# Performance work log

Measured on AMD Instinct MI355X. Metric: run time of the kernel, lower is better.

## Reference

```python
import jax, jax.numpy as jnp
import numpy as np

BATCH_SIZE = 512
N_PARTS = 4
TEMP_FAC = 0.1
D = 4096
EPS = 1e-6


def _static_indices():
    # bs and factor per the n_parts==4, batch_size!=12 branch
    bs = 4 * BATCH_SIZE
    factor = 10 * N_PARTS
    pos = np.arange(bs)
    active = pos[pos % (3 * N_PARTS) < N_PARTS]            # positions that contribute
    # i1..i6 = (pos + k*n_parts) % bs for k = 0..5
    I = (active[:, None] + np.arange(6)[None, :] * N_PARTS) % bs   # (P, 6)
    # denominator indices removed: (pos + k*n_parts) % bs for k = 0..factor*n_parts-1
    offs = (active[:, None] + np.arange(factor * N_PARTS)[None, :] * N_PARTS) % bs
    M = np.ones((active.shape[0], bs), dtype=np.float32)
    M[np.arange(active.shape[0])[:, None], offs] = 0.0     # (P, bs) denominator mask
    return I, M

_I, _M = _static_indices()
# symmetrical-loss pairs: (i1,i2),(i2,i3),(i1,i4),(i4,i5),(i5,i6),(i2,i5),(i3,i6)
_PAIRS = [(0, 1), (1, 2), (0, 3), (3, 4), (4, 5), (1, 4), (2, 5)]


def setup_inputs() -> dict:
    key = jax.random.key(0)
    reg_pred = jax.random.normal(key, (4 * BATCH_SIZE, D), dtype=jnp.float32)
    return {"reg_pred": reg_pred}


def reference(reg_pred):
    I = jnp.asarray(_I)
    M = jnp.asarray(_M)
    norms = jnp.linalg.norm(reg_pred, axis=1)              # (bs,)
    # torch CosineSimilarity: dot / max(||a||*||b||, eps)
    gram = reg_pred @ reg_pred.T                           # (bs, bs)
    S = gram / jnp.maximum(norms[:, None] * norms[None, :], EPS) / TEMP_FAC
    E = jnp.exp(S)                                         # (bs, bs)
    # denominator exp-sums for each anchor role k at each active position p
    Dsum = jnp.einsum('pkb,pb->pk', E[I], M)               # (P, 6)
    total = jnp.float32(0.0)
    for a, b in _PAIRS:
        num = S[I[:, a], I[:, b]]                          # (P,)
        en = jnp.exp(num)
        total = total + jnp.sum(-jnp.log(en / (en + Dsum[:, a]))
                                - jnp.log(en / (en + Dsum[:, b])))
    return total / (6 * BATCH_SIZE)
```

## Files before the change

### kernel.cpp

```cpp
#include <hip/hip_runtime.h>
#include <hip/hip_bf16.h>
#include <stdint.h>

#define NROWS 2048
#define DIM   4096
#define NACT  684
#define INV_TEMP 10.0f
#define NPANEL 32
#define NTILE64 528
#define NK 64
#define FP8_SCALE 16.0f
#define OUT_SCALE (INV_TEMP / 256.0f)

#define WAITCNT_VM0   0x0F70
#define WAITCNT_VM4   0x0F74
#define WAITCNT_VM8   0x0F78

typedef __attribute__((ext_vector_type(4))) float floatx4;
typedef __attribute__((ext_vector_type(16))) float floatx16;
typedef __attribute__((ext_vector_type(4))) int intx4;
typedef __attribute__((ext_vector_type(8))) int intx8;
typedef __attribute__((ext_vector_type(8))) short shortx8;
typedef __attribute__((ext_vector_type(8))) unsigned short ushortx8;

static __device__ __forceinline__ unsigned short f32_to_bf16(float f) {
  union { float f; unsigned int u; } v; v.f = f;
  unsigned int u = v.u;
  unsigned int r = u + 0x7fffu + ((u >> 16) & 1u);
  return (unsigned short)(r >> 16);
}
static __device__ __forceinline__ float bf16_to_f32(unsigned short u) {
  union { unsigned int u; float f; } v; v.u = ((unsigned int)u) << 16;
  return v.f;
}
static __device__ __forceinline__ unsigned short f32_to_f16(float f) {
  _Float16 h = (_Float16)f;
  union { _Float16 h; unsigned short u; } v; v.h = h;
  return v.u;
}
static __device__ __forceinline__ float f16_to_f32(unsigned short u) {
  union { unsigned short u; _Float16 h; } v; v.u = u;
  return (float)v.h;
}

__global__ __launch_bounds__(256) void k_normconv_fp8(const float* __restrict__ X,
                                                      unsigned char* __restrict__ Yq,
                                                      float* __restrict__ T,
                                                      float* __restrict__ out) {
  const int row = blockIdx.x;
  if (threadIdx.x == 0) T[row] = 0.f;
  if (row == 0 && threadIdx.x == 64) *out = 0.f;
  const float4* xr = (const float4*)(X + (size_t)row * DIM);
  float4 v[4];
  float s = 0.f;
#pragma unroll
  for (int t = 0; t < 4; t++) {
    float4 w = xr[threadIdx.x + t * 256];
    v[t] = w;
    s += w.x * w.x + w.y * w.y + w.z * w.z + w.w * w.w;
  }
#pragma unroll
  for (int off = 32; off > 0; off >>= 1) s += __shfl_down(s, off, 64);
  __shared__ float wsum[4];
  if ((threadIdx.x & 63) == 0) wsum[threadIdx.x >> 6] = s;
  __syncthreads();
  const float total = wsum[0] + wsum[1] + wsum[2] + wsum[3];
  const float sc = FP8_SCALE / fmaxf(sqrtf(total), 1e-30f);
  unsigned int* yr = (unsigned int*)(Yq + (size_t)row * DIM);
#pragma unroll
  for (int t = 0; t < 4; t++) {
    float4 w = v[t];
    unsigned int r0 = __builtin_amdgcn_cvt_pk_fp8_f32(w.x * sc, w.y * sc, 0, false);
    r0 = __builtin_amdgcn_cvt_pk_fp8_f32(w.z * sc, w.w * sc, r0, true);
    yr[threadIdx.x + t * 256] = r0;
  }
}

__global__ __launch_bounds__(256) void k_gemm_full(const unsigned char* __restrict__ Yq,
                                                   unsigned short* __restrict__ S,
                                                   float* __restrict__ T) {
  __shared__ __attribute__((aligned(16))) unsigned char lds[6 * 8192];
  const int bid0 = blockIdx.x;
  const int t = (bid0 & 7) * 66 + (bid0 >> 3);
  int ti = 0, rem = t;
  while (rem >= NPANEL - ti) { rem -= NPANEL - ti; ti++; }
  const int tj = ti + rem;
  const int gr = ti * 64;
  const int gc = tj * 64;

  const int tid  = threadIdx.x;
  const int lane = tid & 63;
  const int wave = tid >> 6;
  const int wr = wave >> 1;
  const int wc = wave & 1;

  floatx16 acc = {0.f, 0.f, 0.f, 0.f, 0.f, 0.f, 0.f, 0.f,
                  0.f, 0.f, 0.f, 0.f, 0.f, 0.f, 0.f, 0.f};

  const int r2  = tid >> 2;
  const int c16 = tid & 3;
  const unsigned int swst = (unsigned)(((r2 >> 1) & 3) << 4);
  const unsigned int colst = ((unsigned)(c16 << 4)) ^ swst;
  const unsigned char* gA = Yq + (size_t)(gr + r2) * DIM + colst;
  const unsigned char* gB = Yq + (size_t)(gc + r2) * DIM + colst;

#define ISSUE(st, koff)                                                                  \
  do {                                                                                   \
    __builtin_amdgcn_global_load_lds(                                                    \
        (const __attribute__((address_space(1))) void*)(gA + (koff)),                    \
        (__attribute__((address_space(3))) void*)(lds + (st) * 8192 + tid * 16),         \
        16, 0, 0);                                                                       \
    __builtin_amdgcn_global_load_lds(                                                    \
        (const __attribute__((address_space(1))) void*)(gB + (koff)),                    \
        (__attribute__((address_space(3))) void*)(lds + (st) * 8192 + 4096 + tid * 16),  \
        16, 0, 0);                                                                       \
  } while (0)

#define COMPUTE(st)                                                                      \
  do {                                                                                   \
    const unsigned char* bA = lds + (st) * 8192;                                         \
    const unsigned char* bB = bA + 4096;                                                 \
    const unsigned int c0 = (unsigned)((lane >> 5) << 5);                                \
    const int rA = wr * 32 + (lane & 31);                                                \
    const int rB = wc * 32 + (lane & 31);                                                \
    const unsigned int swA = (unsigned)(((rA >> 1) & 3) << 4);                           \
    const unsigned int swB = (unsigned)(((rB >> 1) & 3) << 4);                           \
    const unsigned char* baseA = bA + rA * 64;                                           \
    const unsigned char* baseB = bB + rB * 64;                                           \
    intx4 alo = *(const intx4*)(baseA + (c0 ^ swA));                                     \
    intx4 ahi = *(const intx4*)(baseA + ((c0 ^ swA) ^ 16u));                             \
    intx4 blo = *(const intx4*)(baseB + (c0 ^ swB));                                     \
    intx4 bhi = *(const intx4*)(baseB + ((c0 ^ swB) ^ 16u));                             \
    intx8 af, bf;                                                                        \
    af[0] = alo[0]; af[1] = alo[1]; af[2] = alo[2]; af[3] = alo[3];                      \
    af[4] = ahi[0]; af[5] = ahi[1]; af[6] = ahi[2]; af[7] = ahi[3];                      \
    bf[0] = blo[0]; bf[1] = blo[1]; bf[2] = blo[2]; bf[3] = blo[3];                      \
    bf[4] = bhi[0]; bf[5] = bhi[1]; bf[6] = bhi[2]; bf[7] = bhi[3];                      \
    acc = __builtin_amdgcn_mfma_scale_f32_32x32x64_f8f6f4(                               \
        af, bf, acc, 0, 0, 0, 0x7F7F7F7F, 0, 0x7F7F7F7F);                                \
  } while (0)

  ISSUE(0, 0);
  ISSUE(1, 64);
  ISSUE(2, 128);
  ISSUE(3, 192);
#pragma unroll
  for (int p = 0; p < 32; p++) {
    const int a = (2 * p) % 6;
    if (p < 30) {
      const int na = (2 * p + 4) % 6;
      ISSUE(na, (2 * p + 4) * 64);
      ISSUE(na + 1, (2 * p + 5) * 64);
      __builtin_amdgcn_s_waitcnt(WAITCNT_VM8);
    } else if (p == 30) {
      __builtin_amdgcn_s_waitcnt(WAITCNT_VM4);
    } else {
      __builtin_amdgcn_s_waitcnt(WAITCNT_VM0);
    }
    __builtin_amdgcn_sched_barrier(0);
    __builtin_amdgcn_s_barrier();
    __builtin_amdgcn_s_setprio(1);
    COMPUTE(a);
    COMPUTE(a + 1);
    __builtin_amdgcn_s_setprio(0);
    if (p < 31) {
      __builtin_amdgcn_s_barrier();
      __builtin_amdgcn_sched_barrier(0);
    }
  }

#undef ISSUE
#undef COMPUTE

  unsigned short* tile16 = (unsigned short*)lds;
  float* tileE   = (float*)(lds + 8448);
  float* colpart = (float*)(lds + 25088);
  __syncthreads();

  {
    const int col = wc * 32 + (lane & 31);
    float evsum = 0.f;
#pragma unroll
    for (int i = 0; i < 16; i++) {
      const int row = wr * 32 + (i & 3) + 8 * (i >> 2) + 4 * (lane >> 5);
      const float v = acc[i] * OUT_SCALE;
      const float ev = __expf(v);
      tile16[row * 66 + col] = f32_to_f16(v);
      tileE[row * 65 + col] = ev;
      evsum += ev;
    }
    evsum += __shfl_xor(evsum, 32, 64);
    if (lane < 32) colpart[wr * 64 + col] = evsum;
  }
  __syncthreads();

  if (tid < 64) atomicAdd(&T[gc + tid], colpart[tid] + colpart[64 + tid]);

  {
    const int r = tid >> 2, seg = tid & 3;
    const unsigned int* q = (const unsigned int*)tile16 + (r * 33 + seg * 8);
    uint4 w0, w1;
    w0.x = q[0]; w0.y = q[1]; w0.z = q[2]; w0.w = q[3];
    w1.x = q[4]; w1.y = q[5]; w1.z = q[6]; w1.w = q[7];
    uint4* dst = (uint4*)(S + (size_t)(gr + r) * NROWS + gc + seg * 16);
    dst[0] = w0; dst[1] = w1;
  }

  if (ti != tj) {
    if (tid < 64) {
      float rs = 0.f;
#pragma unroll 8
      for (int c = 0; c < 64; c++) rs += tileE[tid * 65 + c];
      atomicAdd(&T[gr + tid], rs);
    }
    {
      const int c = tid >> 2, seg = tid & 3;
      unsigned short tmp[16];
#pragma unroll
      for (int k = 0; k < 16; k++) tmp[k] = tile16[(seg * 16 + k) * 66 + c];
      uint4 w0, w1;
      w0.x = (unsigned int)tmp[0]  | ((unsigned int)tmp[1]  << 16);
      w0.y = (unsigned int)tmp[2]  | ((unsigned int)tmp[3]  << 16);
      w0.z = (unsigned int)tmp[4]  | ((unsigned int)tmp[5]  << 16);
      w0.w = (unsigned int)tmp[6]  | ((unsigned int)tmp[7]  << 16);
      w1.x = (unsigned int)tmp[8]  | ((unsigned int)tmp[9]  << 16);
      w1.y = (unsigned int)tmp[10] | ((unsigned int)tmp[11] << 16);
      w1.z = (unsigned int)tmp[12] | ((unsigned int)tmp[13] << 16);
      w1.w = (unsigned int)tmp[14] | ((unsigned int)tmp[15] << 16);
      uint4* dst = (uint4*)(S + (size_t)(gc + c) * NROWS + gr + seg * 16);
      dst[0] = w0; dst[1] = w1;
    }
  }
}

__global__ __launch_bounds__(384) void k_tail(const unsigned short* __restrict__ S,
                                              const float* __restrict__ T,
                                              float* __restrict__ out) {
  __shared__ float ds_s[6];
  const int p = blockIdx.x;
  const int a = 12 * (p >> 2) + (p & 3);
  const int tid = threadIdx.x;
  const int k = tid >> 6;
  const int lane = tid & 63;
  const int row = (a + 4 * k) & (NROWS - 1);
  const int m = a >> 2;
  const int c = a & 3;
  const uint2* sr = (const uint2*)(S + (size_t)row * NROWS);
  float s = 0.f;
  {
    uint2 v0 = sr[(m + lane) & 511];
    uint2 v1 = sr[(m + 64 + lane) & 511];
    unsigned short e0 = (c < 2) ? (unsigned short)(v0.x >> (16 * c))
                                : (unsigned short)(v0.y >> (16 * (c - 2)));
    unsigned short e1 = (c < 2) ? (unsigned short)(v1.x >> (16 * c))
                                : (unsigned short)(v1.y >> (16 * (c - 2)));
    s += __expf(f16_to_f32(e0)) + __expf(f16_to_f32(e1));
    if (lane < 32) {
      uint2 v2 = sr[(m + 128 + lane) & 511];
      unsigned short e2 = (c < 2) ? (unsigned short)(v2.x >> (16 * c))
                                  : (unsigned short)(v2.y >> (16 * (c - 2)));
      s += __expf(f16_to_f32(e2));
    }
  }
#pragma unroll
  for (int off = 32; off > 0; off >>= 1) s += __shfl_down(s, off, 64);
  if (lane == 0) ds_s[k] = T[row] - s;
  __syncthreads();

  float r = 0.f;
  if (tid < 7) {
    const int pa[7] = {0, 1, 0, 3, 4, 1, 2};
    const int pb[7] = {1, 2, 3, 4, 5, 4, 5};
    const int ra = (a + 4 * pa[tid]) & (NROWS - 1);
    const int rb = (a + 4 * pb[tid]) & (NROWS - 1);
    const float num = f16_to_f32(S[(size_t)ra * NROWS + rb]);
    const float en = __expf(num);
    r = __logf(en + ds_s[pa[tid]]) + __logf(en + ds_s[pb[tid]]) - 2.f * num;
  }
  if (tid < 64) {
    r += __shfl_down(r, 4, 64);
    r += __shfl_down(r, 2, 64);
    r += __shfl_down(r, 1, 64);
    if (tid == 0) atomicAdd(out, r * (1.0f / (6.0f * 512.0f)));
  }
}

__global__ __launch_bounds__(256) void k_normconv(const float* __restrict__ X,
                                                  unsigned short* __restrict__ Y) {
  const int row = blockIdx.x;
  const float4* xr = (const float4*)(X + (size_t)row * DIM);
  float4 v[4];
  float s = 0.f;
#pragma unroll
  for (int t = 0; t < 4; t++) {
    float4 w = xr[threadIdx.x + t * 256];
    v[t] = w;
    s += w.x * w.x + w.y * w.y + w.z * w.z + w.w * w.w;
  }
#pragma unroll
  for (int off = 32; off > 0; off >>= 1) s += __shfl_down(s, off, 64);
  __shared__ float wsum[4];
  if ((threadIdx.x & 63) == 0) wsum[threadIdx.x >> 6] = s;
  __syncthreads();
  const float total = wsum[0] + wsum[1] + wsum[2] + wsum[3];
  const float inv = 1.0f / fmaxf(sqrtf(total), 1e-30f);
  ushort4* yr = (ushort4*)(Y + (size_t)row * DIM);
#pragma unroll
  for (int t = 0; t < 4; t++) {
    float4 w = v[t];
    ushort4 o;
    o.x = f32_to_bf16(w.x * inv);
    o.y = f32_to_bf16(w.y * inv);
    o.z = f32_to_bf16(w.z * inv);
    o.w = f32_to_bf16(w.w * inv);
    yr[threadIdx.x + t * 256] = o;
  }
}

__global__ __launch_bounds__(256) void k_gemm(const unsigned short* __restrict__ Y,
                                              float* __restrict__ S) {
  __shared__ __attribute__((aligned(16))) unsigned short sA[128 * 32];
  __shared__ __attribute__((aligned(16))) unsigned short sB[128 * 32];
  const int tid  = threadIdx.x;
  const int lane = tid & 63;
  const int wave = tid >> 6;
  const int wr = wave >> 1;
  const int wc = wave & 1;
  const int row0 = blockIdx.y * 128;
  const int col0 = blockIdx.x * 128;

  floatx4 zero = {0.f, 0.f, 0.f, 0.f};
  floatx4 acc[4][4];
#pragma unroll
  for (int i = 0; i < 4; i++)
#pragma unroll
    for (int j = 0; j < 4; j++) acc[i][j] = zero;

  const int sr = tid >> 2;
  const int sc = (tid & 3) * 8;
  const unsigned short* gA0 = Y + (size_t)(row0 + sr) * DIM + sc;
  const unsigned short* gA1 = gA0 + (size_t)64 * DIM;
  const unsigned short* gB0 = Y + (size_t)(col0 + sr) * DIM + sc;
  const unsigned short* gB1 = gB0 + (size_t)64 * DIM;

  const int fr = lane & 15;
  const int fc = (lane >> 4) * 8;

  for (int k0 = 0; k0 < DIM; k0 += 32) {
    __builtin_amdgcn_global_load_lds(
        (const __attribute__((address_space(1))) void*)(gA0 + k0),
        (__attribute__((address_space(3))) void*)(sA + tid * 8), 16, 0, 0);
    __builtin_amdgcn_global_load_lds(
        (const __attribute__((address_space(1))) void*)(gA1 + k0),
        (__attribute__((address_space(3))) void*)(sA + 2048 + tid * 8), 16, 0, 0);
    __builtin_amdgcn_global_load_lds(
        (const __attribute__((address_space(1))) void*)(gB0 + k0),
        (__attribute__((address_space(3))) void*)(sB + tid * 8), 16, 0, 0);
    __builtin_amdgcn_global_load_lds(
        (const __attribute__((address_space(1))) void*)(gB1 + k0),
        (__attribute__((address_space(3))) void*)(sB + 2048 + tid * 8), 16, 0, 0);
    __syncthreads();

    shortx8 af[4], bf[4];
#pragma unroll
    for (int mi = 0; mi < 4; mi++)
      af[mi] = *(const shortx8*)(sA + (wr * 64 + mi * 16 + fr) * 32 + fc);
#pragma unroll
    for (int ni = 0; ni < 4; ni++)
      bf[ni] = *(const shortx8*)(sB + (wc * 64 + ni * 16 + fr) * 32 + fc);
#pragma unroll
    for (int mi = 0; mi < 4; mi++)
#pragma unroll
      for (int ni = 0; ni < 4; ni++)
        acc[mi][ni] = __builtin_amdgcn_mfma_f32_16x16x32_bf16(af[mi], bf[ni], acc[mi][ni], 0, 0, 0);
    __syncthreads();
  }

  const int cc  = lane & 15;
  const int cr4 = (lane >> 4) * 4;
#pragma unroll
  for (int mi = 0; mi < 4; mi++) {
    const int row = row0 + wr * 64 + mi * 16 + cr4;
#pragma unroll
    for (int ni = 0; ni < 4; ni++) {
      const int col = col0 + wc * 64 + ni * 16 + cc;
      float* dst = S + (size_t)row * NROWS + col;
#pragma unroll
      for (int r = 0; r < 4; r++) dst[(size_t)r * NROWS] = acc[mi][ni][r] * INV_TEMP;
    }
  }
}

__global__ __launch_bounds__(256) void k_rowsum(const float* __restrict__ S,
                                                float* __restrict__ T) {
  const int row = blockIdx.x;
  const float* sr = S + (size_t)row * NROWS;
  float s = 0.f;
  for (int b = threadIdx.x; b < NROWS; b += 256) s += __expf(sr[b]);
#pragma unroll
  for (int off = 32; off > 0; off >>= 1) s += __shfl_down(s, off, 64);
  __shared__ float wsum[4];
  if ((threadIdx.x & 63) == 0) wsum[threadIdx.x >> 6] = s;
  __syncthreads();
  if (threadIdx.x == 0) T[row] = wsum[0] + wsum[1] + wsum[2] + wsum[3];
}

__global__ __launch_bounds__(64) void k_dsum(const float* __restrict__ S,
                                             const float* __restrict__ T,
                                             float* __restrict__ Ds) {
  const int p = blockIdx.x;
  const int k = blockIdx.y;
  const int a = 12 * (p >> 2) + (p & 3);
  const int lane = threadIdx.x;
  const int row = (a + 4 * k) & (NROWS - 1);
  const int m = a >> 2;
  const int c = a & 3;
  const float4* sr4 = (const float4*)(S + (size_t)row * NROWS);
  float s = 0.f;
  {
    float4 v0 = sr4[(m + lane) & 511];
    float4 v1 = sr4[(m + 64 + lane) & 511];
    float e0 = c == 0 ? v0.x : c == 1 ? v0.y : c == 2 ? v0.z : v0.w;
    float e1 = c == 0 ? v1.x : c == 1 ? v1.y : c == 2 ? v1.z : v1.w;
    s += __expf(e0) + __expf(e1);
    if (lane < 32) {
      float4 v2 = sr4[(m + 128 + lane) & 511];
      float e2 = c == 0 ? v2.x : c == 1 ? v2.y : c == 2 ? v2.z : v2.w;
      s += __expf(e2);
    }
  }
#pragma unroll
  for (int off = 32; off > 0; off >>= 1) s += __shfl_down(s, off, 64);
  if (lane == 0) Ds[p * 6 + k] = T[row] - s;
}

__global__ __launch_bounds__(256) void k_final(const float* __restrict__ S,
                                               const float* __restrict__ Ds,
                                               float* __restrict__ out) {
  const int pa[7] = {0, 1, 0, 3, 4, 1, 2};
  const int pb[7] = {1, 2, 3, 4, 5, 4, 5};
  const int idx = blockIdx.x * 256 + threadIdx.x;
  float s = 0.f;
  if (idx < NACT * 7) {
    const int p = idx / 7;
    const int q = idx - p * 7;
    const int a0 = 12 * (p >> 2) + (p & 3);
    const int ra = (a0 + 4 * pa[q]) & (NROWS - 1);
    const int rb = (a0 + 4 * pb[q]) & (NROWS - 1);
    const float num = S[(size_t)ra * NROWS + rb];
    const float en = __expf(num);
    s = __logf(en + Ds[p * 6 + pa[q]]) + __logf(en + Ds[p * 6 + pb[q]]) - 2.f * num;
  }
#pragma unroll
  for (int off = 32; off > 0; off >>= 1) s += __shfl_down(s, off, 64);
  if ((threadIdx.x & 63) == 0) atomicAdd(out, s * (1.0f / (6.0f * 512.0f)));
}

extern "C" void kernel_launch(void* const* d_in, const int* in_sizes, int n_in,
                              void* d_out, int out_size, void* d_ws, size_t ws_size,
                              hipStream_t stream) {
  const float* X = (const float*)d_in[0];
  char* ws = (char*)d_ws;
  float* out = (float*)d_out;

  const size_t pOff = (size_t)32 * 1024 * 1024;
  const size_t needA = pOff + 8192 + 256;

  if (ws_size >= needA) {
    unsigned char* Yq = (unsigned char*)ws;
    unsigned short* S16 = (unsigned short*)(ws + (size_t)16 * 1024 * 1024);
    float* T  = (float*)(ws + pOff);
    hipLaunchKernelGGL(k_normconv_fp8, dim3(NROWS), dim3(256), 0, stream, X, Yq, T, out);
    hipLaunchKernelGGL(k_gemm_full, dim3(NTILE64), dim3(256), 0, stream, Yq, S16, T);
    hipLaunchKernelGGL(k_tail, dim3(NACT), dim3(384), 0, stream, S16, T, out);
  } else {
    unsigned short* Y = (unsigned short*)ws;
    float* S = (float*)(ws + (size_t)16 * 1024 * 1024);
    float* T  = (float*)(ws + pOff);
    float* Ds = (float*)(ws + pOff + 8192);
    hipMemsetAsync(out, 0, sizeof(float), stream);
    hipLaunchKernelGGL(k_normconv, dim3(NROWS), dim3(256), 0, stream, X, Y);
    hipLaunchKernelGGL(k_gemm, dim3(16, 16), dim3(256), 0, stream, Y, S);
    hipLaunchKernelGGL(k_rowsum, dim3(NROWS), dim3(256), 0, stream, S, T);
    hipLaunchKernelGGL(k_dsum, dim3(NACT, 6), dim3(64), 0, stream, S, T, Ds);
    hipLaunchKernelGGL(k_final, dim3((NACT * 7 + 255) / 256), dim3(256), 0, stream, S, Ds, out);
  }
}
```

Before: 107.7 us.

## Fuse masked denominator sums and numerators into GEMM epilogue, drop S matrix

The GEMM epilogue no longer writes the fp16 similarity matrix S (and its transpose) to global memory. It now accumulates the masked window exp-sums per anchor role straight into a small WS buffer with atomics, and scatters the few needed numerator similarities into a NUM buffer. The tail kernel that re-read S rows is replaced by a tiny final kernel that reads only T, WS and NUM. This removes about 8MB of writes plus the gather reads, at the cost of extra epilogue branching, divisions and more atomics per tile.

```diff
diff --git a/kernel.cpp b/kernel.cpp
--- a/kernel.cpp
+++ b/kernel.cpp
@@ -43,13 +43,37 @@
   return (float)v.h;
 }
 
+static __device__ __forceinline__ void num_store(float* __restrict__ NUM, int R, int delta,
+                                                 float v) {
+  if (delta == 4) {
+    const int qs[4]  = {0, 1, 3, 4};
+    const int pas[4] = {0, 1, 3, 4};
+#pragma unroll
+    for (int u = 0; u < 4; u++) {
+      const int aa = (R - 4 * pas[u]) & (NROWS - 1);
+      if (aa % 12 < 4) NUM[((aa / 12) * 4 + (aa % 12)) * 7 + qs[u]] = v;
+    }
+  } else {
+    const int qs[3]  = {2, 5, 6};
+    const int pas[3] = {0, 1, 2};
+#pragma unroll
+    for (int u = 0; u < 3; u++) {
+      const int aa = (R - 4 * pas[u]) & (NROWS - 1);
+      if (aa % 12 < 4) NUM[((aa / 12) * 4 + (aa % 12)) * 7 + qs[u]] = v;
+    }
+  }
+}
+
 __global__ __launch_bounds__(256) void k_normconv_fp8(const float* __restrict__ X,
                                                       unsigned char* __restrict__ Yq,
                                                       float* __restrict__ T,
+                                                      float* __restrict__ WS,
                                                       float* __restrict__ out) {
   const int row = blockIdx.x;
   if (threadIdx.x == 0) T[row] = 0.f;
   if (row == 0 && threadIdx.x == 64) *out = 0.f;
+  if (row < NACT && threadIdx.x >= 192 && threadIdx.x < 198)
+    WS[row * 6 + (threadIdx.x - 192)] = 0.f;
   const float4* xr = (const float4*)(X + (size_t)row * DIM);
   float4 v[4];
   float s = 0.f;
@@ -77,8 +101,9 @@
 }
 
 __global__ __launch_bounds__(256) void k_gemm_full(const unsigned char* __restrict__ Yq,
-                                                   unsigned short* __restrict__ S,
-                                                   float* __restrict__ T) {
+                                                   float* __restrict__ T,
+                                                   float* __restrict__ WS,
+                                                   float* __restrict__ NUM) {
   __shared__ __attribute__((aligned(16))) unsigned char lds[6 * 8192];
   const int bid0 = blockIdx.x;
   const int t = (bid0 & 7) * 66 + (bid0 >> 3);
@@ -172,9 +197,8 @@
 #undef ISSUE
 #undef COMPUTE
 
-  unsigned short* tile16 = (unsigned short*)lds;
-  float* tileE   = (float*)(lds + 8448);
-  float* colpart = (float*)(lds + 25088);
+  float* tileE   = (float*)lds;
+  float* colpart = (float*)(lds + 16640);
   __syncthreads();
 
   {
@@ -185,104 +209,93 @@
       const int row = wr * 32 + (i & 3) + 8 * (i >> 2) + 4 * (lane >> 5);
       const float v = acc[i] * OUT_SCALE;
       const float ev = __expf(v);
-      tile16[row * 66 + col] = f32_to_f16(v);
       tileE[row * 65 + col] = ev;
       evsum += ev;
+      const int D = (gc + col - gr - row) & (NROWS - 1);
+      if (D == 4 || D == 12) num_store(NUM, gr + row, D, v);
+      if (ti != tj && (D == 2044 || D == 2036)) num_store(NUM, gc + col, 2048 - D, v);
     }
     evsum += __shfl_xor(evsum, 32, 64);
     if (lane < 32) colpart[wr * 64 + col] = evsum;
   }
   __syncthreads();
 
-  if (tid < 64) atomicAdd(&T[gc + tid], colpart[tid] + colpart[64 + tid]);
-
-  {
-    const int r = tid >> 2, seg = tid & 3;
-    const unsigned int* q = (const unsigned int*)tile16 + (r * 33 + seg * 8);
-    uint4 w0, w1;
-    w0.x = q[0]; w0.y = q[1]; w0.z = q[2]; w0.w = q[3];
-    w1.x = q[4]; w1.y = q[5]; w1.z = q[6]; w1.w = q[7];
-    uint4* dst = (uint4*)(S + (size_t)(gr + r) * NROWS + gc + seg * 16);
-    dst[0] = w0; dst[1] = w1;
-  }
-
-  if (ti != tj) {
-    if (tid < 64) {
+  if (tid < 64) {
+    const int R = gr + tid;
+#pragma unroll
+    for (int k = 0; k < 6; k++) {
+      const int aa = (R - 4 * k) & (NROWS - 1);
+      if (aa % 12 < 4) {
+        const int p2 = (aa / 12) * 4 + (aa % 12);
+        const int c = aa & 3;
+        const int j0 = ((gc >> 2) - (aa >> 2)) & 511;
+        float w = 0.f;
+#pragma unroll
+        for (int i2 = 0; i2 < 16; i2++) {
+          const int j = j0 + i2;
+          if (j < 160 || j >= 512) w += tileE[tid * 65 + 4 * i2 + c];
+        }
+        atomicAdd(&WS[p2 * 6 + k], w);
+      }
+    }
+  } else if (tid < 128) {
+    if (ti != tj) {
+      const int col = tid - 64;
+      const int R = gc + col;
+#pragma unroll
+      for (int k = 0; k < 6; k++) {
+        const int aa = (R - 4 * k) & (NROWS - 1);
+        if (aa % 12 < 4) {
+          const int p2 = (aa / 12) * 4 + (aa % 12);
+          const int c = aa & 3;
+          const int j0 = ((gr >> 2) - (aa >> 2)) & 511;
+          float w = 0.f;
+#pragma unroll
+          for (int i2 = 0; i2 < 16; i2++) {
+            const int j = j0 + i2;
+            if (j < 160 || j >= 512) w += tileE[(4 * i2 + c) * 65 + col];
+          }
+          atomicAdd(&WS[p2 * 6 + k], w);
+        }
+      }
+    }
+  } else if (tid < 192) {
+    if (ti != tj) {
+      const int r = tid - 128;
       float rs = 0.f;
 #pragma unroll 8
-      for (int c = 0; c < 64; c++) rs += tileE[tid * 65 + c];
-      atomicAdd(&T[gr + tid], rs);
-    }
-    {
-      const int c = tid >> 2, seg = tid & 3;
-      unsigned short tmp[16];
-#pragma unroll
-      for (int k = 0; k < 16; k++) tmp[k] = tile16[(seg * 16 + k) * 66 + c];
-      uint4 w0, w1;
-      w0.x = (unsigned int)tmp[0]  | ((unsigned int)tmp[1]  << 16);
-      w0.y = (unsigned int)tmp[2]  | ((unsigned int)tmp[3]  << 16);
-      w0.z = (unsigned int)tmp[4]  | ((unsigned int)tmp[5]  << 16);
-      w0.w = (unsigned int)tmp[6]  | ((unsigned int)tmp[7]  << 16);
-      w1.x = (unsigned int)tmp[8]  | ((unsigned int)tmp[9]  << 16);
-      w1.y = (unsigned int)tmp[10] | ((unsigned int)tmp[11] << 16);
-      w1.z = (unsigned int)tmp[12] | ((unsigned int)tmp[13] << 16);
-      w1.w = (unsigned int)tmp[14] | ((unsigned int)tmp[15] << 16);
-      uint4* dst = (uint4*)(S + (size_t)(gc + c) * NROWS + gr + seg * 16);
-      dst[0] = w0; dst[1] = w1;
-    }
-  }
-}
-
-__global__ __launch_bounds__(384) void k_tail(const unsigned short* __restrict__ S,
-                                              const float* __restrict__ T,
-                                              float* __restrict__ out) {
-  __shared__ float ds_s[6];
-  const int p = blockIdx.x;
-  const int a = 12 * (p >> 2) + (p & 3);
-  const int tid = threadIdx.x;
-  const int k = tid >> 6;
-  const int lane = tid & 63;
-  const int row = (a + 4 * k) & (NROWS - 1);
-  const int m = a >> 2;
-  const int c = a & 3;
-  const uint2* sr = (const uint2*)(S + (size_t)row * NROWS);
+      for (int c = 0; c < 64; c++) rs += tileE[r * 65 + c];
+      atomicAdd(&T[gr + r], rs);
+    }
+  } else {
+    const int c = tid - 192;
+    atomicAdd(&T[gc + c], colpart[c] + colpart[64 + c]);
+  }
+}
+
+__global__ __launch_bounds__(256) void k_finalA(const float* __restrict__ NUM,
+                                                const float* __restrict__ WS,
+                                                const float* __restrict__ T,
+                                                float* __restrict__ out) {
+  const int pa[7] = {0, 1, 0, 3, 4, 1, 2};
+  const int pb[7] = {1, 2, 3, 4, 5, 4, 5};
+  const int idx = blockIdx.x * 256 + threadIdx.x;
   float s = 0.f;
-  {
-    uint2 v0 = sr[(m + lane) & 511];
-    uint2 v1 = sr[(m + 64 + lane) & 511];
-    unsigned short e0 = (c < 2) ? (unsigned short)(v0.x >> (16 * c))
-                                : (unsigned short)(v0.y >> (16 * (c - 2)));
-    unsigned short e1 = (c < 2) ? (unsigned short)(v1.x >> (16 * c))
-                                : (unsigned short)(v1.y >> (16 * (c - 2)));
-    s += __expf(f16_to_f32(e0)) + __expf(f16_to_f32(e1));
-    if (lane < 32) {
-      uint2 v2 = sr[(m + 128 + lane) & 511];
-      unsigned short e2 = (c < 2) ? (unsigned short)(v2.x >> (16 * c))
-                                  : (unsigned short)(v2.y >> (16 * (c - 2)));
-      s += __expf(f16_to_f32(e2));
-    }
+  if (idx < NACT * 7) {
+    const int p = idx / 7;
+    const int q = idx - p * 7;
+    const int a0 = 12 * (p >> 2) + (p & 3);
+    const int ra = (a0 + 4 * pa[q]) & (NROWS - 1);
+    const int rb = (a0 + 4 * pb[q]) & (NROWS - 1);
+    const float dsA = T[ra] - WS[p * 6 + pa[q]];
+    const float dsB = T[rb] - WS[p * 6 + pb[q]];
+    const float num = NUM[idx];
+    const float en = __expf(num);
+    s = __logf(en + dsA) + __logf(en + dsB) - 2.f * num;
   }
 #pragma unroll
   for (int off = 32; off > 0; off >>= 1) s += __shfl_down(s, off, 64);
-  if (lane == 0) ds_s[k] = T[row] - s;
-  __syncthreads();
-
-  float r = 0.f;
-  if (tid < 7) {
-    const int pa[7] = {0, 1, 0, 3, 4, 1, 2};
-    const int pb[7] = {1, 2, 3, 4, 5, 4, 5};
-    const int ra = (a + 4 * pa[tid]) & (NROWS - 1);
-    const int rb = (a + 4 * pb[tid]) & (NROWS - 1);
-    const float num = f16_to_f32(S[(size_t)ra * NROWS + rb]);
-    const float en = __expf(num);
-    r = __logf(en + ds_s[pa[tid]]) + __logf(en + ds_s[pb[tid]]) - 2.f * num;
-  }
-  if (tid < 64) {
-    r += __shfl_down(r, 4, 64);
-    r += __shfl_down(r, 2, 64);
-    r += __shfl_down(r, 1, 64);
-    if (tid == 0) atomicAdd(out, r * (1.0f / (6.0f * 512.0f)));
-  }
+  if ((threadIdx.x & 63) == 0) atomicAdd(out, s * (1.0f / (6.0f * 512.0f)));
 }
 
 __global__ __launch_bounds__(256) void k_normconv(const float* __restrict__ X,
@@ -464,15 +477,17 @@
   float* out = (float*)d_out;
 
   const size_t pOff = (size_t)32 * 1024 * 1024;
-  const size_t needA = pOff + 8192 + 256;
+  const size_t needA = pOff + 8192 + 24576 + 24576;
 
   if (ws_size >= needA) {
     unsigned char* Yq = (unsigned char*)ws;
-    unsigned short* S16 = (unsigned short*)(ws + (size_t)16 * 1024 * 1024);
-    float* T  = (float*)(ws + pOff);
-    hipLaunchKernelGGL(k_normconv_fp8, dim3(NROWS), dim3(256), 0, stream, X, Yq, T, out);
-    hipLaunchKernelGGL(k_gemm_full, dim3(NTILE64), dim3(256), 0, stream, Yq, S16, T);
-    hipLaunchKernelGGL(k_tail, dim3(NACT), dim3(384), 0, stream, S16, T, out);
+    float* T   = (float*)(ws + pOff);
+    float* WS  = (float*)(ws + pOff + 8192);
+    float* NUM = (float*)(ws + pOff + 8192 + 24576);
+    hipLaunchKernelGGL(k_normconv_fp8, dim3(NROWS), dim3(256), 0, stream, X, Yq, T, WS, out);
+    hipLaunchKernelGGL(k_gemm_full, dim3(NTILE64), dim3(256), 0, stream, Yq, T, WS, NUM);
+    hipLaunchKernelGGL(k_finalA, dim3((NACT * 7 + 255) / 256), dim3(256), 0, stream,
+                       NUM, WS, T, out);
   } else {
     unsigned short* Y = (unsigned short*)ws;
     float* S = (float*)(ws + (size_t)16 * 1024 * 1024);
```

Result: faster. 105.2 us (-2.3%).
